# Kernel optimization log

Hardware: AMD Instinct MI355X
Metric: run time of the kernel (lower is better)

## Reference

```python
import jax, jax.numpy as jnp
import numpy as np

B, C, H = 2, 32, 64  # batch, concat channels, cube side (H==W==D required by attaxis reshapes)
Ch = C // 2


def _conv3d(x, w, b, pad):
    # conv3d block = Conv3d + bias + ReLU (n=1 conv block)
    y = jax.lax.conv_general_dilated(x, w, (1, 1, 1), [(p, p) for p in pad],
                                     dimension_numbers=('NCDHW', 'OIDHW', 'NCDHW'))
    return jax.nn.relu(y + b[None, :, None, None, None])


def setup_inputs():
    key = jax.random.key(0)
    ks = jax.random.split(key, 16)
    w = lambda k, s: jax.random.normal(k, s, dtype=jnp.float32) * 0.05
    z = lambda n: jnp.zeros((n,), jnp.float32)
    return {
        'x1': jax.random.normal(ks[0], (B, Ch, H, H, H), jnp.float32),
        'x2': jax.random.normal(ks[1], (B, Ch, H, H, H), jnp.float32),
        'w_red': w(ks[2], (1, C, 3, 3, 3)), 'b_red': z(1),
        'w_cx': w(ks[3], (1, 1, 1, 1, H)), 'b_cx': z(1),
        'w_cy': w(ks[4], (1, 1, 1, H, 1)), 'b_cy': z(1),
        'w_cz': w(ks[5], (1, 1, H, 1, 1)), 'b_cz': z(1),
        'w_sp1': w(ks[6], (1, 1, 1, 1, 1)), 'b_sp1': z(1),
        'w_sp3': w(ks[7], (1, 1, 3, 3, 3)), 'b_sp3': z(1),
        'w_sp5a': w(ks[8], (1, 1, 3, 3, 3)), 'b_sp5a': z(1),
        'w_sp5b': w(ks[9], (1, 1, 3, 3, 3)), 'b_sp5b': z(1),
        'w_fus': w(ks[10], (C, 1, 3, 3, 3)), 'b_fus': z(C),
        'w_c1': w(ks[11], (Ch, Ch, 3, 3, 3)), 'b_c1': z(Ch),
        'w_c2': w(ks[12], (Ch, Ch, 3, 3, 3)), 'b_c2': z(Ch),
    }


def _kernal(x, w_cx, b_cx, w_cy, b_cy, w_cz, b_cz,
            w_sp1, b_sp1, w_sp3, b_sp3, w_sp5a, b_sp5a, w_sp5b, b_sp5b):
    b, c, h, ww, d = x.shape
    # xyzaxis: axis-collapsing convs, then attaxis attention over S = h*w tokens
    q = _conv3d(x, w_cx, b_cx, (0, 0, 0))                        # [b,1,h,w,1]
    k = jnp.swapaxes(_conv3d(x, w_cy, b_cy, (0, 0, 0)), 3, 4)    # [b,1,h,d,1]
    v = jnp.swapaxes(_conv3d(x, w_cz, b_cz, (0, 0, 0)), 2, 4)    # [b,1,d,w,1]
    S = h * ww
    Q = q.reshape(b, S, 1)
    K = k.reshape(b, S, 1)
    V = v.reshape(b, S, 1)
    qk = jax.nn.softmax(jnp.einsum('bsc,btc->bst', Q, K), axis=-1)  # [b,S,S]
    xyz = jnp.einsum('bst,btc->bsc', qk, V).reshape(b, 1, h, ww, 1)
    # multi-branch convs + full-tensor att(sp1, sp3, sp5)
    sp1 = _conv3d(x, w_sp1, b_sp1, (0, 0, 0))
    sp3 = _conv3d(x, w_sp3, b_sp3, (1, 1, 1))
    sp5 = _conv3d(_conv3d(x, w_sp5a, b_sp5a, (1, 1, 1)), w_sp5b, b_sp5b, (1, 1, 1))
    attn = jnp.matmul(jax.nn.softmax(jnp.matmul(sp1, sp3), axis=-1), sp5)
    return xyz + attn + x  # xyz broadcasts over last dim


def reference(x1, x2, w_red, b_red, w_cx, b_cx, w_cy, b_cy, w_cz, b_cz,
              w_sp1, b_sp1, w_sp3, b_sp3, w_sp5a, b_sp5a, w_sp5b, b_sp5b,
              w_fus, b_fus, w_c1, b_c1, w_c2, b_c2):
    x = jnp.concatenate([x1, x2], axis=1)                 # [B,C,H,H,H]
    hx = _conv3d(x, w_red, b_red, (1, 1, 1))              # DenseSP.reducePool -> 1 channel
    hx = _kernal(hx, w_cx, b_cx, w_cy, b_cy, w_cz, b_cz,
                 w_sp1, b_sp1, w_sp3, b_sp3, w_sp5a, b_sp5a, w_sp5b, b_sp5b)
    sp = jax.nn.sigmoid(_conv3d(hx, w_fus, b_fus, (1, 1, 1)) + x)  # DenseSP output
    x = sp * x + x
    c = x.shape[1] // 2
    y1 = _conv3d(x[:, :c] + x1, w_c1, b_c1, (1, 1, 1))
    y2 = _conv3d(x[:, c:] + x2, w_c2, b_c2, (1, 1, 1))
    return (y1, y2)
```

## Files before the change

kernel.cpp:

```cpp
#include <hip/hip_runtime.h>

#define DEVFN static __device__ __forceinline__

constexpr int HHH = 262144;
constexpr int HH  = 4096;
constexpr int SP  = 20;

typedef __attribute__((ext_vector_type(8))) short short8;
typedef __attribute__((ext_vector_type(4))) float f32x4;
typedef __attribute__((address_space(1))) void GV;
typedef __attribute__((address_space(3))) void LV;

#define OFF_HX   ((size_t)0)
#define OFF_SP3  (OFF_HX   + 2*(size_t)HHH)
#define OFF_SP5A (OFF_SP3  + 2*(size_t)HHH)
#define OFF_SP5B (OFF_SP5A + 2*(size_t)HHH)
#define OFF_HXO  (OFF_SP5B + 2*(size_t)HHH)
#define OFF_Q    (OFF_HXO  + 2*(size_t)HHH)
#define OFF_K    (OFF_Q    + 2*(size_t)HH)
#define OFF_V    (OFF_K    + 2*(size_t)HH)
#define OFF_XYZ  (OFF_V    + 2*(size_t)HH)
#define OFF_KM   (OFF_XYZ  + 2*(size_t)HH)
#define OFF_Z    (OFF_KM   + 16)
#define OFF_WPRE (OFF_Z    + 32*(size_t)HHH)
#define OFF_ZPAD (OFF_WPRE + 7168)

DEVFN unsigned short f2bf(float f)
{
    unsigned u = __builtin_bit_cast(unsigned, f);
    u += 0x7fffu + ((u >> 16) & 1u);
    return (unsigned short)(u >> 16);
}

DEVFN void stage20(const float* __restrict__ src, float* __restrict__ tile,
                   int z0, int y0, int x0, int tid)
{
    for (int i = tid; i < 1800; i += 256) {
        int lz = i / 180;
        int r  = i - lz * 180;
        int ly = r / 18;
        int lx = r - ly * 18;
        int gz = z0 - 1 + lz, gy = y0 - 1 + ly, gx = x0 - 1 + lx;
        float v = 0.f;
        if ((unsigned)(gz | gy | gx) < 64u)
            v = src[(gz * 64 + gy) * 64 + gx];
        tile[(lz * 10 + ly) * SP + lx] = v;
    }
}

DEVFN void loadnb(const float* __restrict__ tile, int tz, int ty, int txg,
                  float4* pa, float2* pb)
{
#pragma unroll
    for (int dz = 0; dz < 3; ++dz) {
#pragma unroll
        for (int dy = 0; dy < 3; ++dy) {
            const float* row = &tile[((tz + dz) * 10 + (ty + dy)) * SP + txg * 4];
            pa[dz * 3 + dy] = *(const float4*)row;
            pb[dz * 3 + dy] = *(const float2*)(row + 4);
        }
    }
}

DEVFN float4 conv27r(const float4* pa, const float2* pb,
                     const float* __restrict__ wc, float4 acc)
{
#pragma unroll
    for (int t = 0; t < 9; ++t) {
        float w0 = wc[3 * t], w1 = wc[3 * t + 1], w2 = wc[3 * t + 2];
        float4 p = pa[t];
        float2 q = pb[t];
        acc.x = fmaf(p.x, w0, fmaf(p.y, w1, fmaf(p.z, w2, acc.x)));
        acc.y = fmaf(p.y, w0, fmaf(p.z, w1, fmaf(p.w, w2, acc.y)));
        acc.z = fmaf(p.z, w0, fmaf(p.w, w1, fmaf(q.x, w2, acc.z)));
        acc.w = fmaf(p.w, w0, fmaf(q.x, w1, fmaf(q.y, w2, acc.w)));
    }
    return acc;
}

__global__ __launch_bounds__(256) void k_wprep(
    const float* __restrict__ w1, const float* __restrict__ w2,
    unsigned short* __restrict__ wpre, float* __restrict__ zpad)
{
    int item = blockIdx.x * 256 + threadIdx.x;
    if (item >= 1792) {
        if (item < 1796) zpad[item - 1792] = 0.f;
        return;
    }
    int half = item / 896;
    int rem  = item - half * 896;
    int t = rem >> 6, lane = rem & 63;
    const float* w = half ? w2 : w1;
    int co = lane & 15, g = lane >> 4;
    int cihalf = g & 1, tapsel = g >> 1;
    int tap = 2 * t + tapsel;
    unsigned v[4] = {0u, 0u, 0u, 0u};
    if (tap < 27) {
#pragma unroll
        for (int p = 0; p < 4; ++p) {
            unsigned short lo = f2bf(w[(co * 16 + cihalf * 8 + 2 * p) * 27 + tap]);
            unsigned short hi = f2bf(w[(co * 16 + cihalf * 8 + 2 * p + 1) * 27 + tap]);
            v[p] = (unsigned)lo | ((unsigned)hi << 16);
        }
    }
    uint4 pk = {v[0], v[1], v[2], v[3]};
    ((uint4*)wpre)[item] = pk;
}

__global__ __launch_bounds__(256) void k_conv_red32(
    const float* __restrict__ x1, const float* __restrict__ x2,
    const float* __restrict__ w, const float* __restrict__ bias,
    const float* __restrict__ zpad, float* __restrict__ hx)
{
    __shared__ __align__(16) float buf[2][2000];
    const int tid = threadIdx.x;
    const int tz = tid >> 5, ty = (tid >> 2) & 7, txg = tid & 3;
    const int bz = blockIdx.z;
    const int b = bz >> 3, z0 = (bz & 7) * 8;
    const int y0 = blockIdx.y * 8, x0 = blockIdx.x * 16;

    int gofs[8];
    bool act[8], inb[8];
#pragma unroll
    for (int k = 0; k < 8; ++k) {
        int i = tid + k * 256;
        act[k] = (i < 2000);
        inb[k] = false; gofs[k] = 0;
        if (act[k]) {
            int lz = i / 200, r = i - lz * 200, ly = r / 20, lx = r - ly * 20;
            int gz = z0 - 1 + lz, gy = y0 - 1 + ly, gx = x0 - 1 + lx;
            if (lx < 18 && (unsigned)(gz | gy | gx) < 64u) {
                inb[k] = true;
                gofs[k] = (gz * 64 + gy) * 64 + gx;
            }
        }
    }

#define DMACH(c, bi)                                                            \
    {                                                                           \
        const float* s_ = ((c) < 16 ? x1 : x2) + (size_t)(b * 16 + ((c) & 15)) * HHH; \
        char* lb_ = (char*)&buf[bi][0];                                         \
        _Pragma("unroll")                                                       \
        for (int k = 0; k < 8; ++k) {                                           \
            int i_ = tid + k * 256;                                             \
            if (act[k]) {                                                       \
                const char* g_ = inb[k] ? (const char*)(s_ + gofs[k])           \
                                        : (const char*)zpad;                    \
                __builtin_amdgcn_global_load_lds((GV*)g_,                       \
                    (LV*)(lb_ + (size_t)i_ * 4), 4, 0, 0);                      \
            }                                                                   \
        }                                                                       \
    }

    DMACH(0, 0);
    __syncthreads();

    float4 acc = {0.f, 0.f, 0.f, 0.f};
    for (int c = 0; c < 32; ++c) {
        if (c + 1 < 32) DMACH(c + 1, (c + 1) & 1);
        const float* tb = buf[c & 1];
        const float* wc = w + c * 27;
        float4 pa[9]; float2 pb[9];
        loadnb(tb, tz, ty, txg, pa, pb);
        acc = conv27r(pa, pb, wc, acc);
        __syncthreads();
    }
#undef DMACH

    float bv = bias[0];
    float4 o = {fmaxf(acc.x + bv, 0.f), fmaxf(acc.y + bv, 0.f),
                fmaxf(acc.z + bv, 0.f), fmaxf(acc.w + bv, 0.f)};
    size_t oidx = (size_t)b * HHH + ((size_t)(z0 + tz) * 64 + (y0 + ty)) * 64 + (x0 + txg * 4);
    *(float4*)&hx[oidx] = o;
}

__global__ __launch_bounds__(256) void k_conv1ch(
    const float* __restrict__ in, const float* __restrict__ w,
    const float* __restrict__ bias, float* __restrict__ outp)
{
    __shared__ __align__(16) float tile[2000];
    const int tid = threadIdx.x;
    const int tz = tid >> 5, ty = (tid >> 2) & 7, txg = tid & 3;
    const int b  = blockIdx.z >> 3;
    const int z0 = (blockIdx.z & 7) * 8, y0 = blockIdx.y * 8, x0 = blockIdx.x * 16;

    stage20(in + (size_t)b * HHH, tile, z0, y0, x0, tid);
    __syncthreads();
    float4 pa[9]; float2 pb[9];
    loadnb(tile, tz, ty, txg, pa, pb);
    float4 acc = {0.f, 0.f, 0.f, 0.f};
    acc = conv27r(pa, pb, w, acc);
    float bv = bias[0];
    float4 o = {fmaxf(acc.x + bv, 0.f), fmaxf(acc.y + bv, 0.f),
                fmaxf(acc.z + bv, 0.f), fmaxf(acc.w + bv, 0.f)};
    size_t oidx = (size_t)b * HHH + ((size_t)(z0 + tz) * 64 + (y0 + ty)) * 64 + (x0 + txg * 4);
    *(float4*)&outp[oidx] = o;
}

__global__ __launch_bounds__(256) void k_conv1ch_dual(
    const float* __restrict__ in,
    const float* __restrict__ wa, const float* __restrict__ ba, float* __restrict__ oa,
    const float* __restrict__ wb, const float* __restrict__ bb, float* __restrict__ ob)
{
    __shared__ __align__(16) float tile[2000];
    const int tid = threadIdx.x;
    const int tz = tid >> 5, ty = (tid >> 2) & 7, txg = tid & 3;
    const int b  = blockIdx.z >> 3;
    const int z0 = (blockIdx.z & 7) * 8, y0 = blockIdx.y * 8, x0 = blockIdx.x * 16;

    stage20(in + (size_t)b * HHH, tile, z0, y0, x0, tid);
    __syncthreads();
    float4 pa[9]; float2 pb[9];
    loadnb(tile, tz, ty, txg, pa, pb);
    float4 zero = {0.f, 0.f, 0.f, 0.f};
    float4 aA = conv27r(pa, pb, wa, zero);
    float4 aB = conv27r(pa, pb, wb, zero);
    float bva = ba[0], bvb = bb[0];
    float4 ra = {fmaxf(aA.x + bva, 0.f), fmaxf(aA.y + bva, 0.f),
                 fmaxf(aA.z + bva, 0.f), fmaxf(aA.w + bva, 0.f)};
    float4 rb = {fmaxf(aB.x + bvb, 0.f), fmaxf(aB.y + bvb, 0.f),
                 fmaxf(aB.z + bvb, 0.f), fmaxf(aB.w + bvb, 0.f)};
    size_t oidx = (size_t)b * HHH + ((size_t)(z0 + tz) * 64 + (y0 + ty)) * 64 + (x0 + txg * 4);
    *(float4*)&oa[oidx] = ra;
    *(float4*)&ob[oidx] = rb;
}

__global__ __launch_bounds__(256) void k_qk(
    const float* __restrict__ hx,
    const float* __restrict__ wq, const float* __restrict__ bq,
    const float* __restrict__ wk, const float* __restrict__ bk,
    float* __restrict__ Q, float* __restrict__ K)
{
    const int bi = blockIdx.x;
    const float* src = hx + (size_t)bi * HH;
    const int tid = threadIdx.x;
    const int j = tid >> 2, q = tid & 3;

    float a = 0.f;
    const float4* sv = (const float4*)(src + j * 64 + q * 16);
#pragma unroll
    for (int k = 0; k < 4; ++k) {
        float4 vv = sv[k];
        a = fmaf(vv.x, wq[q * 16 + k * 4 + 0], a);
        a = fmaf(vv.y, wq[q * 16 + k * 4 + 1], a);
        a = fmaf(vv.z, wq[q * 16 + k * 4 + 2], a);
        a = fmaf(vv.w, wq[q * 16 + k * 4 + 3], a);
    }
    a += __shfl_xor(a, 1); a += __shfl_xor(a, 2);

    float c = 0.f;
#pragma unroll
    for (int jj = 0; jj < 16; ++jj)
        c = fmaf(src[(q * 16 + jj) * 64 + j], wk[q * 16 + jj], c);
    c += __shfl_xor(c, 1); c += __shfl_xor(c, 2);

    if (q == 0) {
        Q[(size_t)bi * 64 + j] = fmaxf(a + bq[0], 0.f);
        K[(size_t)bi * 64 + j] = fmaxf(c + bk[0], 0.f);
    }
}

__global__ __launch_bounds__(256) void k_v(
    const float* __restrict__ hx, const float* __restrict__ wv,
    const float* __restrict__ bv, float* __restrict__ V)
{
    const int bt = blockIdx.x;
    const int b = bt >> 6, t = bt & 63;
    const int tid = threadIdx.x;
    const int j = tid >> 2, q = tid & 3;
    const float* src = hx + (size_t)b * HHH + (size_t)j * 64 + t;
    float a = 0.f;
#pragma unroll
    for (int k = 0; k < 16; ++k) {
        int i = q * 16 + k;
        a = fmaf(src[(size_t)i * HH], wv[i], a);
    }
    a += __shfl_xor(a, 1); a += __shfl_xor(a, 2);
    if (q == 0)
        V[(size_t)b * HH + t * 64 + j] = fmaxf(a + bv[0], 0.f);
}

__global__ void k_kmax(const float* __restrict__ K, float* __restrict__ kmax)
{
    __shared__ float red[256];
    int b = blockIdx.x;
    float m = -1e30f;
    for (int u = threadIdx.x; u < 4096; u += 256) m = fmaxf(m, K[b * 4096 + u]);
    red[threadIdx.x] = m;
    __syncthreads();
    for (int s = 128; s > 0; s >>= 1) {
        if (threadIdx.x < s) red[threadIdx.x] = fmaxf(red[threadIdx.x], red[threadIdx.x + s]);
        __syncthreads();
    }
    if (threadIdx.x == 0) kmax[b] = red[0];
}

__global__ __launch_bounds__(256) void k_xyz(
    const float* __restrict__ Q, const float* __restrict__ K,
    const float* __restrict__ V, const float* __restrict__ kmax,
    float* __restrict__ xyz)
{
    __shared__ float pden[4][64];
    __shared__ float pnum[4][64];
    const int b = blockIdx.y;
    const int chunk = blockIdx.x;
    const int lane = threadIdx.x & 63;
    const int wv = __builtin_amdgcn_readfirstlane(threadIdx.x >> 6);
    const int s = chunk * 64 + lane;
    const float qv = Q[b * 4096 + s];
    const float m = qv * kmax[b];
    const float* Kp = K + b * 4096 + wv * 1024;
    const float* Vp = V + b * 4096 + wv * 1024;
    float den = 0.f, num = 0.f;
#pragma unroll 4
    for (int u = 0; u < 1024; ++u) {
        float e = __expf(fmaf(qv, Kp[u], -m));
        den += e;
        num = fmaf(e, Vp[u], num);
    }
    pden[wv][lane] = den;
    pnum[wv][lane] = num;
    __syncthreads();
    if (threadIdx.x < 64) {
        float d = pden[0][lane] + pden[1][lane] + pden[2][lane] + pden[3][lane];
        float n = pnum[0][lane] + pnum[1][lane] + pnum[2][lane] + pnum[3][lane];
        xyz[b * 4096 + s] = n / d;
    }
}

DEVFN void mac16(const float4* __restrict__ base, int vb, float a, float* acc)
{
    float4 q0 = base[vb], q1 = base[vb + 1], q2 = base[vb + 2], q3 = base[vb + 3];
    float qq[16] = {q0.x, q0.y, q0.z, q0.w, q1.x, q1.y, q1.z, q1.w,
                    q2.x, q2.y, q2.z, q2.w, q3.x, q3.y, q3.z, q3.w};
#pragma unroll
    for (int k = 0; k < 16; ++k) acc[k] = fmaf(a, qq[k], acc[k]);
}

__global__ __launch_bounds__(256) void k_attn(
    const float* __restrict__ hx, const float* __restrict__ sp3,
    const float* __restrict__ sp5, const float* __restrict__ xyz,
    const float* __restrict__ w_sp1, const float* __restrict__ b_sp1,
    float* __restrict__ hxo)
{
    __shared__ __align__(16) float s1[64 * 65];
    __shared__ __align__(16) float s3[4096];
    __shared__ __align__(16) float s5[4096];
    const int tid = threadIdx.x;
    const int bi = blockIdx.x;
    const size_t off = (size_t)bi * HH;
    const float w1 = w_sp1[0], bb = b_sp1[0];
    for (int idx = tid; idx < 4096; idx += 256) {
        float hv = hx[off + idx];
        s1[(idx >> 6) * 65 + (idx & 63)] = fmaxf(fmaf(w1, hv, bb), 0.f);
        s3[idx] = sp3[off + idx];
        s5[idx] = sp5[off + idx];
    }
    __syncthreads();
    const int j = tid >> 2, g = tid & 3, t0 = g * 16;
    float m[16];
#pragma unroll
    for (int k = 0; k < 16; ++k) m[k] = 0.f;
    const float4* s3v = (const float4*)s3;
    for (int r = 0; r < 64; ++r) {
        float a = s1[j * 65 + r];
        mac16(s3v, r * 16 + (t0 >> 2), a, m);
    }
    float mx = m[0];
#pragma unroll
    for (int k = 1; k < 16; ++k) mx = fmaxf(mx, m[k]);
    mx = fmaxf(mx, __shfl_xor(mx, 1));
    mx = fmaxf(mx, __shfl_xor(mx, 2));
    float e[16];
    float sum = 0.f;
#pragma unroll
    for (int k = 0; k < 16; ++k) { e[k] = __expf(m[k] - mx); sum += e[k]; }
    sum += __shfl_xor(sum, 1);
    sum += __shfl_xor(sum, 2);
    const float inv = 1.f / sum;
    __syncthreads();
#pragma unroll
    for (int k = 0; k < 16; ++k) s1[j * 65 + t0 + k] = e[k] * inv;
    __syncthreads();
    float acc[16];
#pragma unroll
    for (int k = 0; k < 16; ++k) acc[k] = 0.f;
    const float4* s5v = (const float4*)s5;
    for (int r = 0; r < 64; ++r) {
        float a = s1[j * 65 + r];
        mac16(s5v, r * 16 + (t0 >> 2), a, acc);
    }
    const float xv = xyz[(size_t)(bi >> 6) * HH + (size_t)(bi & 63) * 64 + j];
    const size_t ob = off + (size_t)j * 64 + t0;
#pragma unroll
    for (int k = 0; k < 16; ++k)
        hxo[ob + k] = xv + acc[k] + hx[ob + k];
}

DEVFN float zcalc(float gg, float bf, float xv)
{
    float t = fmaxf(gg + bf, 0.f) + xv;
    float s = 1.f / (1.f + __expf(-t));
    return xv * (s + 2.f);
}

__global__ __launch_bounds__(256) void k_fuse_half(
    const float* __restrict__ hxo, const float* __restrict__ x1,
    const float* __restrict__ x2, const float* __restrict__ w_fus,
    const float* __restrict__ b_fus, unsigned short* __restrict__ Zb)
{
    __shared__ __align__(16) float tile[2000];
    const int tid = threadIdx.x;
    const int tz = tid >> 5, ty = (tid >> 2) & 7, txg = tid & 3;
    const int bz = blockIdx.z;
    const int zt = bz & 7, bh = bz >> 3;
    const int b = bh >> 1, half = bh & 1;
    const int z0 = zt * 8, y0 = blockIdx.y * 8, x0 = blockIdx.x * 16;

    stage20(hxo + (size_t)b * HHH, tile, z0, y0, x0, tid);
    __syncthreads();
    float4 pa[9]; float2 pb[9];
    loadnb(tile, tz, ty, txg, pa, pb);

    const size_t vox = ((size_t)(z0 + tz) * 64 + (y0 + ty)) * 64 + (x0 + txg * 4);
    const float* xbase = (half ? x2 : x1) + (size_t)(b * 16) * HHH + vox;
    const float* wbase = w_fus + (half * 16) * 27;
    const float* bbase = b_fus + half * 16;

    unsigned zp[4][8];
#pragma unroll
    for (int cc = 0; cc < 16; ++cc) {
        float4 zero = {0.f, 0.f, 0.f, 0.f};
        float4 g = conv27r(pa, pb, wbase + cc * 27, zero);
        float4 xv = *(const float4*)(xbase + (size_t)cc * HHH);
        float bf = bbase[cc];
        unsigned short z0v = f2bf(zcalc(g.x, bf, xv.x));
        unsigned short z1v = f2bf(zcalc(g.y, bf, xv.y));
        unsigned short z2v = f2bf(zcalc(g.z, bf, xv.z));
        unsigned short z3v = f2bf(zcalc(g.w, bf, xv.w));
        int p = cc >> 1;
        if ((cc & 1) == 0) {
            zp[0][p] = z0v; zp[1][p] = z1v; zp[2][p] = z2v; zp[3][p] = z3v;
        } else {
            zp[0][p] |= (unsigned)z0v << 16; zp[1][p] |= (unsigned)z1v << 16;
            zp[2][p] |= (unsigned)z2v << 16; zp[3][p] |= (unsigned)z3v << 16;
        }
    }
    unsigned short* zo = Zb + ((size_t)bh * HHH + vox) * 16;
#pragma unroll
    for (int v = 0; v < 4; ++v) {
        uint4 lo = {zp[v][0], zp[v][1], zp[v][2], zp[v][3]};
        uint4 hi = {zp[v][4], zp[v][5], zp[v][6], zp[v][7]};
        *(uint4*)(zo + v * 16)     = lo;
        *(uint4*)(zo + v * 16 + 8) = hi;
    }
}

__global__ __launch_bounds__(512) void k_convc_mfma(
    const unsigned short* __restrict__ Zb,
    const unsigned short* __restrict__ wpre,
    const float* __restrict__ b1, const float* __restrict__ b2,
    const float* __restrict__ zpad,
    float* __restrict__ out)
{
    __shared__ __align__(16) unsigned short tile[1800 * 16 + 384];
    const int tid = threadIdx.x;
    const int lane = tid & 63;
    const int wvid = tid >> 6;
    const int bz = blockIdx.z;
    const int b = bz >> 4, half = (bz >> 3) & 1, z0 = (bz & 7) * 8;
    const int y0 = blockIdx.y * 8, x0 = blockIdx.x * 16;
    const float* bias = half ? b2 : b1;

    const int g = lane >> 4;
    const int cihalf = g & 1;
    const int tapsel = g >> 1;

    short8 wf[14];
    const short8* wp = (const short8*)wpre + (half * 14) * 64 + lane;
#pragma unroll
    for (int t = 0; t < 14; ++t) wf[t] = wp[t * 64];

    float bfrag[4];
#pragma unroll
    for (int r = 0; r < 4; ++r) bfrag[r] = bias[g * 4 + r];

    const unsigned short* zsrc = Zb + (size_t)(b * 2 + half) * HHH * 16;
    const char* zp = (const char*)zpad;
    char* lbase = (char*)tile;
    for (int it = 0; it < 7; ++it) {
        int i = it * 512 + tid;
        int pos = i >> 1, h = i & 1;
        int lz = pos / 180;
        int r2 = pos - lz * 180;
        int ly = r2 / 18, lx = r2 - ly * 18;
        int gz = z0 - 1 + lz, gy = y0 - 1 + ly, gx = x0 - 1 + lx;
        const char* gsrc = ((unsigned)(gz | gy | gx) < 64u)
            ? (const char*)(zsrc + (((size_t)(gz * 64 + gy)) * 64 + gx) * 16 + h * 8)
            : zp;
        __builtin_amdgcn_global_load_lds((GV*)gsrc, (LV*)(lbase + (size_t)i * 16),
                                         16, 0, 0);
    }
    if (wvid == 0) {
        int i = 3584 + tid;
        const char* gsrc = zp;
        if (i < 3600) {
            int pos = i >> 1, h = i & 1;
            int lz = pos / 180;
            int r2 = pos - lz * 180;
            int ly = r2 / 18, lx = r2 - ly * 18;
            int gz = z0 - 1 + lz, gy = y0 - 1 + ly, gx = x0 - 1 + lx;
            if ((unsigned)(gz | gy | gx) < 64u)
                gsrc = (const char*)(zsrc + (((size_t)(gz * 64 + gy)) * 64 + gx) * 16 + h * 8);
        }
        __builtin_amdgcn_global_load_lds((GV*)gsrc, (LV*)(lbase + (size_t)i * 16),
                                         16, 0, 0);
    }
    __syncthreads();

    int offs[14];
#pragma unroll
    for (int t = 0; t < 14; ++t) {
        int tap = 2 * t + tapsel;
        int tcl = tap < 27 ? tap : 26;
        int dz = tcl / 9, rr = tcl - dz * 9;
        int dy = rr / 3, dx = rr - dy * 3;
        offs[t] = (((dz * 10 + dy) * 18 + dx + (lane & 15)) << 5) + (cihalf << 4);
    }

    const char* tb = (const char*)tile;
    for (int rr = 0; rr < 8; ++rr) {
        int rowid = wvid * 8 + rr;
        int zr = rowid >> 3, yr = rowid & 7;
        int rbase = ((zr * 10 + yr) * 18) << 5;
        f32x4 acc = {0.f, 0.f, 0.f, 0.f};
        f32x4 acc2 = {0.f, 0.f, 0.f, 0.f};
#pragma unroll
        for (int t = 0; t < 14; t += 2) {
            short8 bf0 = *(const short8*)(tb + (rbase + offs[t]));
            acc = __builtin_amdgcn_mfma_f32_16x16x32_bf16(wf[t], bf0, acc, 0, 0, 0);
            short8 bf1 = *(const short8*)(tb + (rbase + offs[t + 1]));
            acc2 = __builtin_amdgcn_mfma_f32_16x16x32_bf16(wf[t + 1], bf1, acc2, 0, 0, 0);
        }
        size_t vox = ((size_t)(z0 + zr) * 64 + (y0 + yr)) * 64 + x0 + (lane & 15);
        float* ob = out + (size_t)half * (2 * 16 * (size_t)HHH) + (size_t)(b * 16) * HHH + vox;
#pragma unroll
        for (int r = 0; r < 4; ++r) {
            float v = acc[r] + acc2[r] + bfrag[r];
            ob[(size_t)(g * 4 + r) * HHH] = fmaxf(v, 0.f);
        }
    }
}

extern "C" void kernel_launch(void* const* d_in, const int* in_sizes, int n_in,
                              void* d_out, int out_size, void* d_ws, size_t ws_size,
                              hipStream_t stream)
{
    const float* x1     = (const float*)d_in[0];
    const float* x2     = (const float*)d_in[1];
    const float* w_red  = (const float*)d_in[2];
    const float* b_red  = (const float*)d_in[3];
    const float* w_cx   = (const float*)d_in[4];
    const float* b_cx   = (const float*)d_in[5];
    const float* w_cy   = (const float*)d_in[6];
    const float* b_cy   = (const float*)d_in[7];
    const float* w_cz   = (const float*)d_in[8];
    const float* b_cz   = (const float*)d_in[9];
    const float* w_sp1  = (const float*)d_in[10];
    const float* b_sp1  = (const float*)d_in[11];
    const float* w_sp3  = (const float*)d_in[12];
    const float* b_sp3  = (const float*)d_in[13];
    const float* w_sp5a = (const float*)d_in[14];
    const float* b_sp5a = (const float*)d_in[15];
    const float* w_sp5b = (const float*)d_in[16];
    const float* b_sp5b = (const float*)d_in[17];
    const float* w_fus  = (const float*)d_in[18];
    const float* b_fus  = (const float*)d_in[19];
    const float* w_c1   = (const float*)d_in[20];
    const float* b_c1   = (const float*)d_in[21];
    const float* w_c2   = (const float*)d_in[22];
    const float* b_c2   = (const float*)d_in[23];

    float* ws  = (float*)d_ws;
    float* out = (float*)d_out;

    float* HX   = ws + OFF_HX;
    float* SP3  = ws + OFF_SP3;
    float* SP5A = ws + OFF_SP5A;
    float* SP5B = ws + OFF_SP5B;
    float* HXO  = ws + OFF_HXO;
    float* Qb   = ws + OFF_Q;
    float* Kb   = ws + OFF_K;
    float* Vb   = ws + OFF_V;
    float* XYZb = ws + OFF_XYZ;
    float* KM   = ws + OFF_KM;
    unsigned short* Zb   = (unsigned short*)(ws + OFF_Z);
    unsigned short* WPRE = (unsigned short*)(ws + OFF_WPRE);
    float* ZPAD = ws + OFF_ZPAD;

    k_wprep    <<<8, 256, 0, stream>>>(w_c1, w_c2, WPRE, ZPAD);
    k_conv_red32<<<dim3(4, 8, 16), 256, 0, stream>>>(x1, x2, w_red, b_red, ZPAD, HX);
    k_conv1ch_dual<<<dim3(4, 8, 16), 256, 0, stream>>>(HX, w_sp3, b_sp3, SP3,
                                                       w_sp5a, b_sp5a, SP5A);
    k_conv1ch  <<<dim3(4, 8, 16), 256, 0, stream>>>(SP5A, w_sp5b, b_sp5b, SP5B);
    k_qk       <<<128, 256, 0, stream>>>(HX, w_cx, b_cx, w_cy, b_cy, Qb, Kb);
    k_v        <<<128, 256, 0, stream>>>(HX, w_cz, b_cz, Vb);
    k_kmax     <<<2, 256, 0, stream>>>(Kb, KM);
    k_xyz      <<<dim3(64, 2), 256, 0, stream>>>(Qb, Kb, Vb, KM, XYZb);
    k_attn     <<<128, 256, 0, stream>>>(HX, SP3, SP5B, XYZb, w_sp1, b_sp1, HXO);
    k_fuse_half<<<dim3(4, 8, 32), 256, 0, stream>>>(HXO, x1, x2, w_fus, b_fus, Zb);
    k_convc_mfma<<<dim3(4, 8, 32), 512, 0, stream>>>(Zb, WPRE, b_c1, b_c2, ZPAD, out);
}
```

Baseline: 211.9 us.

## Triple-buffer channel tiles in reduce conv with partial vmcnt waits

```diff
diff --git a/kernel.cpp b/kernel.cpp
--- a/kernel.cpp
+++ b/kernel.cpp
@@ -112,7 +112,7 @@
     const float* __restrict__ w, const float* __restrict__ bias,
     const float* __restrict__ zpad, float* __restrict__ hx)
 {
-    __shared__ __align__(16) float buf[2][2000];
+    __shared__ __align__(16) float buf[3][2048];
     const int tid = threadIdx.x;
     const int tz = tid >> 5, ty = (tid >> 2) & 7, txg = tid & 3;
     const int bz = blockIdx.z;
@@ -120,13 +120,12 @@
     const int y0 = blockIdx.y * 8, x0 = blockIdx.x * 16;
 
     int gofs[8];
-    bool act[8], inb[8];
+    bool inb[8];
 #pragma unroll
     for (int k = 0; k < 8; ++k) {
         int i = tid + k * 256;
-        act[k] = (i < 2000);
         inb[k] = false; gofs[k] = 0;
-        if (act[k]) {
+        if (i < 2000) {
             int lz = i / 200, r = i - lz * 200, ly = r / 20, lx = r - ly * 20;
             int gz = z0 - 1 + lz, gy = y0 - 1 + ly, gx = x0 - 1 + lx;
             if (lx < 18 && (unsigned)(gz | gy | gx) < 64u) {
@@ -142,28 +141,37 @@
         char* lb_ = (char*)&buf[bi][0];                                         \
         _Pragma("unroll")                                                       \
         for (int k = 0; k < 8; ++k) {                                           \
-            int i_ = tid + k * 256;                                             \
-            if (act[k]) {                                                       \
-                const char* g_ = inb[k] ? (const char*)(s_ + gofs[k])           \
-                                        : (const char*)zpad;                    \
-                __builtin_amdgcn_global_load_lds((GV*)g_,                       \
-                    (LV*)(lb_ + (size_t)i_ * 4), 4, 0, 0);                      \
-            }                                                                   \
+            const char* g_ = inb[k] ? (const char*)(s_ + gofs[k])               \
+                                    : (const char*)zpad;                        \
+            __builtin_amdgcn_global_load_lds((GV*)g_,                           \
+                (LV*)(lb_ + (size_t)(tid + k * 256) * 4), 4, 0, 0);             \
         }                                                                       \
+        __builtin_amdgcn_sched_barrier(0);                                      \
     }
 
     DMACH(0, 0);
-    __syncthreads();
+    DMACH(1, 1);
+    asm volatile("s_waitcnt vmcnt(8)" ::: "memory");
+    __builtin_amdgcn_sched_barrier(0);
+    __builtin_amdgcn_s_barrier();
 
     float4 acc = {0.f, 0.f, 0.f, 0.f};
     for (int c = 0; c < 32; ++c) {
-        if (c + 1 < 32) DMACH(c + 1, (c + 1) & 1);
-        const float* tb = buf[c & 1];
-        const float* wc = w + c * 27;
+        int nb = c + 2;
+        if (nb < 32) DMACH(nb, nb % 3);
+        const float* tb = buf[c % 3];
         float4 pa[9]; float2 pb[9];
         loadnb(tb, tz, ty, txg, pa, pb);
-        acc = conv27r(pa, pb, wc, acc);
-        __syncthreads();
+        acc = conv27r(pa, pb, w + c * 27, acc);
+        if (c + 1 < 32) {
+            if (nb < 32) {
+                asm volatile("s_waitcnt vmcnt(8)" ::: "memory");
+            } else {
+                asm volatile("s_waitcnt vmcnt(0)" ::: "memory");
+            }
+            __builtin_amdgcn_sched_barrier(0);
+            __builtin_amdgcn_s_barrier();
+        }
     }
 #undef DMACH
 
```

Measured after the change: 212.0 us (median of 5 runs). Within noise of the previous version (+0.0%).
